# Performance work log

Hardware: AMD Instinct MI355X
Metric: run time of the kernel (lower is better)

Reference implementation:

```python
import jax, jax.numpy as jnp
import numpy as np

N = 50000      # nodes
E = 800000     # edges (avg degree 16)
F = 6          # input node features
C = 64         # conv_hidden_channels
M = 256        # mlp_hidden_channels
NCLS = 24      # num_classes
EPS = 1e-5     # BatchNorm eps


def _bn(h, g, b):
    # BatchNorm1d in training mode: biased batch stats over the batch axis
    mu = h.mean(axis=0)
    var = ((h - mu) ** 2).mean(axis=0)
    return g * (h - mu) * jax.lax.rsqrt(var + EPS) + b


def _block(x, W, b, g, beta):
    # Lin -> ReLU -> BN  (one MLP block)
    return _bn(jax.nn.relu(x @ W + b), g, beta)


def _edge_conv(x, src, dst, Wa, ba, ga, bea, Wb, bb, gb, beb):
    # EdgeConv: message = MLP([x_i, x_j - x_i]), max-aggregated onto target i
    xi = x[dst]                                   # [E, d]
    xj = x[src]                                   # [E, d]
    e = jnp.concatenate([xi, xj - xi], axis=-1)   # [E, 2d]
    h = _block(_block(e, Wa, ba, ga, bea), Wb, bb, gb, beb)  # [E, C]
    agg = jax.ops.segment_max(h, dst, num_segments=N)        # [N, C]
    return jnp.where(jnp.isfinite(agg), agg, 0.0)  # zero-fill isolated nodes


def setup_inputs() -> dict:
    key = jax.random.key(0)
    ks = jax.random.split(key, 12)

    def w(k, shape, fan_in):
        return jax.random.normal(k, shape, jnp.float32) * (1.0 / np.sqrt(fan_in))

    z = lambda *s: jnp.zeros(s, jnp.float32)
    o = lambda *s: jnp.ones(s, jnp.float32)

    x = jax.random.normal(ks[0], (N, F), jnp.float32)
    edge_index = jax.random.randint(ks[1], (2, E), 0, N, jnp.int32)

    return {
        "x": x,
        # conv1 MLP: Lin(2F,C)+BN, Lin(C,C)+BN
        "W1a": w(ks[2], (2 * F, C), 2 * F), "b1a": z(C), "g1a": o(C), "be1a": z(C),
        "W1b": w(ks[3], (C, C), C),         "b1b": z(C), "g1b": o(C), "be1b": z(C),
        # conv2/conv3 stacked: Lin(2C,C)+BN, Lin(C,C)+BN
        "Wa": w(ks[4], (2, 2 * C, C), 2 * C), "ba": z(2, C), "ga": o(2, C), "bea": z(2, C),
        "Wb": w(ks[5], (2, C, C), C),         "bb": z(2, C), "gb": o(2, C), "beb": z(2, C),
        # lin1: Lin(3C, M)+BN
        "Wl": w(ks[6], (3 * C, M), 3 * C), "bl": z(M), "gl": o(M), "bel": z(M),
        # head: Lin(M, M/4)+BN, Lin(M/4, M/8)+BN, Lin(M/8, NCLS)
        "Wm1": w(ks[7], (M, M // 4), M),      "bm1": z(M // 4), "gm1": o(M // 4), "bem1": z(M // 4),
        "Wm2": w(ks[8], (M // 4, M // 8), M // 4), "bm2": z(M // 8), "gm2": o(M // 8), "bem2": z(M // 8),
        "Wo": w(ks[9], (M // 8, NCLS), M // 8), "bo": z(NCLS),
        "edge_index": edge_index,
    }


def reference(x, W1a, b1a, g1a, be1a, W1b, b1b, g1b, be1b,
              Wa, ba, ga, bea, Wb, bb, gb, beb,
              Wl, bl, gl, bel,
              Wm1, bm1, gm1, bem1, Wm2, bm2, gm2, bem2,
              Wo, bo, edge_index):
    src, dst = edge_index[0], edge_index[1]
    x1 = _edge_conv(x,  src, dst, W1a, b1a, g1a, be1a, W1b, b1b, g1b, be1b)
    x2 = _edge_conv(x1, src, dst, Wa[0], ba[0], ga[0], bea[0], Wb[0], bb[0], gb[0], beb[0])
    x3 = _edge_conv(x2, src, dst, Wa[1], ba[1], ga[1], bea[1], Wb[1], bb[1], gb[1], beb[1])
    h = _block(jnp.concatenate([x1, x2, x3], axis=-1), Wl, bl, gl, bel)
    h = _block(h, Wm1, bm1, gm1, bem1)   # Dropout is identity (eval)
    h = _block(h, Wm2, bm2, gm2, bem2)   # Dropout is identity (eval)
    logits = h @ Wo + bo
    return jax.nn.log_softmax(logits, axis=1)
```

## Files before the change

### kernel.cpp

```cpp
#include <hip/hip_runtime.h>
#include <hip/hip_bf16.h>

#define EPS 1e-5f
typedef unsigned short bfr;
typedef unsigned short hfr;
typedef _Float16 h2v __attribute__((ext_vector_type(2)));
typedef _Float16 f16x8 __attribute__((ext_vector_type(8)));
typedef float f32x4 __attribute__((ext_vector_type(4)));

#if defined(__has_builtin)
#if __has_builtin(__builtin_amdgcn_fdot2)
#define HAS_FDOT2 1
#endif
#endif

static inline int cdiv(int a, int b){ return (a + b - 1) / b; }
static inline int imin(int a, int b){ return a < b ? a : b; }

__device__ __forceinline__ float bf2f(bfr u){ return __uint_as_float((unsigned)u << 16); }
__device__ __forceinline__ bfr f2bf(float f){
  unsigned u = __float_as_uint(f);
  u += 0x7fffu + ((u >> 16) & 1u);
  return (bfr)(u >> 16);
}
__device__ __forceinline__ unsigned pack2bf(float a, float b){
  return (unsigned)f2bf(a) | ((unsigned)f2bf(b) << 16);
}
__device__ __forceinline__ float h2f(hfr u){ _Float16 h; __builtin_memcpy(&h, &u, 2); return (float)h; }
__device__ __forceinline__ hfr f2h(float f){ _Float16 h = (_Float16)f; hfr u; __builtin_memcpy(&u, &h, 2); return u; }
__device__ __forceinline__ unsigned pack2h(float a, float b){
  return (unsigned)f2h(a) | ((unsigned)f2h(b) << 16);
}
__device__ __forceinline__ h2v u2h2(unsigned u){ h2v r; __builtin_memcpy(&r, &u, 4); return r; }
__device__ __forceinline__ unsigned h22u(h2v h){ unsigned u; __builtin_memcpy(&u, &h, 4); return u; }
__device__ __forceinline__ float dot2(h2v a, h2v b, float c){
#ifdef HAS_FDOT2
  return __builtin_amdgcn_fdot2(a, b, c, false);
#else
  return c + (float)a.x * (float)b.x + (float)a.y * (float)b.y;
#endif
}

__global__ __launch_bounds__(256) void detect_kernel(const bfr* __restrict__ xr, int nwords, int* __restrict__ flag){
  int i = threadIdx.x;
  int bad = 0;
  if (i < nwords){
    bfr lo = xr[2 * i];
    int e = (lo >> 7) & 0xFF;
    bool plausible = ((lo & 0x7FFF) == 0) || (e >= 97 && e <= 157);
    bad = plausible ? 0 : 1;
  }
  __shared__ int s[256];
  s[threadIdx.x] = bad; __syncthreads();
  for (int st = 128; st; st >>= 1){
    if (threadIdx.x < st) s[threadIdx.x] += s[threadIdx.x + st];
    __syncthreads();
  }
  if (threadIdx.x == 0) *flag = (s[0] > 32) ? 1 : 0;
}

#define NPAR 31
struct ParamPtrs { const void* p[NPAR]; };
struct ParamOfs  { int off[NPAR + 1]; };

__global__ __launch_bounds__(256) void acvt_batch_kernel(ParamPtrs pp, ParamOfs po,
                                                         float* __restrict__ out, int total,
                                                         const int* __restrict__ flag){
  int g = blockIdx.x * 256 + threadIdx.x;
  if (g >= total) return;
  int isf = *flag;
  int t = 0;
  while (po.off[t + 1] <= g) ++t;
  int i = g - po.off[t];
  out[g] = isf ? ((const float*)pp.p[t])[i] : bf2f(((const bfr*)pp.p[t])[i]);
}

__global__ __launch_bounds__(256) void deg_kernel(const int* __restrict__ dst, int* __restrict__ deg, int E){
  int e = blockIdx.x * 256 + threadIdx.x;
  if (e < E) atomicAdd(&deg[dst[e]], 1);
}

__global__ __launch_bounds__(256) void scan1_kernel(const int* __restrict__ deg, int* __restrict__ locoff,
                                                    int* __restrict__ bsum, int N){
  __shared__ int s[256];
  int i = blockIdx.x * 256 + threadIdx.x;
  int v = (i < N) ? deg[i] : 0;
  s[threadIdx.x] = v; __syncthreads();
  for (int st = 1; st < 256; st <<= 1){
    int u = (threadIdx.x >= st) ? s[threadIdx.x - st] : 0;
    __syncthreads();
    s[threadIdx.x] += u;
    __syncthreads();
  }
  if (i < N) locoff[i] = s[threadIdx.x] - v;
  if (threadIdx.x == 255) bsum[blockIdx.x] = s[255];
}

__global__ __launch_bounds__(256) void scan2_kernel(int* __restrict__ bsum, int nb){
  __shared__ int s[256];
  const int t = threadIdx.x;
  int carry = 0;
  for (int base = 0; base < nb; base += 256){
    int v = (base + t < nb) ? bsum[base + t] : 0;
    s[t] = v; __syncthreads();
    for (int st = 1; st < 256; st <<= 1){
      int u = (t >= st) ? s[t - st] : 0;
      __syncthreads();
      s[t] += u;
      __syncthreads();
    }
    if (base + t < nb) bsum[base + t] = carry + s[t] - v;
    carry += s[255];
    __syncthreads();
  }
}

__global__ __launch_bounds__(256) void scan3_kernel(const int* __restrict__ locoff, const int* __restrict__ bsum,
                                                    int* __restrict__ row_off, int* __restrict__ cur,
                                                    int N, int E){
  int i = blockIdx.x * 256 + threadIdx.x;
  if (i < N){
    int v = locoff[i] + bsum[blockIdx.x];
    row_off[i] = v; cur[i] = v;
  }
  if (i == 0) row_off[N] = E;
}

__global__ __launch_bounds__(256) void scatter_kernel(const int* __restrict__ src, const int* __restrict__ dst,
                                                      int* __restrict__ cur, int* __restrict__ ssrc, int E){
  int e = blockIdx.x * 256 + threadIdx.x;
  if (e < E){
    int d = dst[e];
    int p = atomicAdd(&cur[d], 1);
    ssrc[p] = src[e];
  }
}

template<bool FIRST>
__global__ __launch_bounds__(256) void gemmPQ_kernel(const void* __restrict__ Av, int lda,
                                                     const float* __restrict__ Wa, int d,
                                                     const float* __restrict__ ba,
                                                     hfr* __restrict__ P, hfr* __restrict__ Q, int N){
  __shared__ unsigned WsU[64 * 64];
  const int y = blockIdx.y;
  const int tot = d * 64;
  if (FIRST){
    float* Ws = (float*)WsU;
    for (int i = threadIdx.x; i < tot; i += 256)
      Ws[i] = y ? Wa[tot + i] : (Wa[i] - Wa[tot + i]);
  } else {
    for (int i = threadIdx.x; i < 32 * 64; i += 256){
      int p = i >> 6, c = i & 63;
      int i0 = (2 * p) * 64 + c, i1 = (2 * p + 1) * 64 + c;
      float w0 = y ? Wa[tot + i0] : (Wa[i0] - Wa[tot + i0]);
      float w1 = y ? Wa[tot + i1] : (Wa[i1] - Wa[tot + i1]);
      WsU[i] = pack2h(w0, w1);
    }
  }
  __syncthreads();
  const int row = blockIdx.x * 256 + threadIdx.x;
  if (row >= N) return;
  float acc[64];
#pragma unroll
  for (int c = 0; c < 64; ++c) acc[c] = 0.f;
  if (FIRST){
    const float* Ws = (const float*)WsU;
    const float* Af = (const float*)Av + (size_t)row * lda;
    for (int k = 0; k < d; ++k){
      float a = Af[k];
      const float* wr = Ws + k * 64;
#pragma unroll
      for (int c4 = 0; c4 < 16; ++c4){
        float4 w = *(const float4*)(wr + 4 * c4);
        acc[4*c4+0] += a * w.x; acc[4*c4+1] += a * w.y;
        acc[4*c4+2] += a * w.z; acc[4*c4+3] += a * w.w;
      }
    }
  } else {
    const hfr* Ah = (const hfr*)Av + (size_t)row * lda;
#pragma unroll
    for (int k8 = 0; k8 < 8; ++k8){
      uint4 av = *(const uint4*)(Ah + k8 * 8);
      unsigned pr[4] = {av.x, av.y, av.z, av.w};
#pragma unroll
      for (int pi = 0; pi < 4; ++pi){
        h2v ap = u2h2(pr[pi]);
        const unsigned* wr = WsU + (k8 * 4 + pi) * 64;
#pragma unroll
        for (int c = 0; c < 64; ++c) acc[c] = dot2(ap, u2h2(wr[c]), acc[c]);
      }
    }
  }
  if (!y){
#pragma unroll
    for (int c = 0; c < 64; ++c) acc[c] += ba[c];
  }
  unsigned p[32];
#pragma unroll
  for (int c = 0; c < 64; c += 2) p[c / 2] = pack2h(acc[c], acc[c + 1]);
  hfr* outp = (y ? Q : P) + (size_t)row * 64;
  uint4* op = (uint4*)outp;
#pragma unroll
  for (int i = 0; i < 8; ++i) op[i] = make_uint4(p[4*i], p[4*i+1], p[4*i+2], p[4*i+3]);
}

template<int NOUT, int KSTEPS, bool FOLD, bool PQ>
__global__ __launch_bounds__(256) void mgemm_kernel(const hfr* __restrict__ Ah, int lda,
                                                    const float* __restrict__ Wp0, const float* __restrict__ Wm0, int ldw,
                                                    const float* __restrict__ bias0,
                                                    const float* __restrict__ stats, float cntInv,
                                                    const float* __restrict__ g, const float* __restrict__ be,
                                                    hfr* __restrict__ Ov0, hfr* __restrict__ Ov1, int ldo,
                                                    int nrows, int relu){
  constexpr int K  = KSTEPS * 32;
  constexpr int KP = K + 8;
  constexpr int NT = NOUT / 16;
  __shared__ __align__(16) _Float16 W2T[NOUT * KP];
  __shared__ __align__(16) _Float16 etile[4][16][NOUT + 8];
  __shared__ float aS[FOLD ? K : 1], bbS[FOLD ? K : 1], bsum[FOLD ? 256 : 1];
  __shared__ float bfull[NOUT];
  const int tid = threadIdx.x;
  const int lane = tid & 63;
  const int wib = tid >> 6;
  const float* Wp = Wp0;
  const float* Wm = Wm0;
  const float* bias = bias0;
  hfr* Ov = Ov0;
  int colbase = blockIdx.y * NOUT;
  if (PQ){
    colbase = 0;
    if (blockIdx.y == 1){ Wp = Wp0 + (size_t)K * ldw; Wm = nullptr; bias = nullptr; Ov = Ov1; }
    else { Wm = Wp0 + (size_t)K * ldw; }
  }

  if (FOLD){
    for (int k = tid; k < K; k += 256){
      float mu = stats[k] * cntInv;
      float var = stats[K + k] * cntInv - mu * mu;
      float ai = g[k] * rsqrtf(var + EPS);
      aS[k] = ai; bbS[k] = be[k] - ai * mu;
    }
    __syncthreads();
  }
  for (int i = tid; i < K * NOUT; i += 256){
    int k = i / NOUT, c = i - k * NOUT;
    float w = Wp[(size_t)k * ldw + colbase + c];
    if (Wm) w -= Wm[(size_t)k * ldw + colbase + c];
    if (FOLD) w *= aS[k];
    W2T[c * KP + k] = (_Float16)w;
  }
  if (FOLD){
    constexpr int parts = 256 / NOUT;
    int c = tid % NOUT, p = tid / NOUT;
    float s = 0.f;
    for (int k = p; k < K; k += parts) s += bbS[k] * Wp[(size_t)k * ldw + colbase + c];
    bsum[p * NOUT + c] = s;
    __syncthreads();
    if (tid < NOUT){
      float t = bias[colbase + tid];
#pragma unroll
      for (int pp = 0; pp < parts; ++pp) t += bsum[pp * NOUT + tid];
      bfull[tid] = t;
    }
  } else {
    if (tid < NOUT) bfull[tid] = bias ? bias[colbase + tid] : 0.f;
  }
  __syncthreads();

  f16x8 Bf[KSTEPS][NT];
#pragma unroll
  for (int s = 0; s < KSTEPS; ++s)
#pragma unroll
    for (int t = 0; t < NT; ++t)
      Bf[s][t] = *(const f16x8*)&W2T[(t * 16 + (lane & 15)) * KP + s * 32 + (lane >> 4) * 8];
  float bc[NT];
#pragma unroll
  for (int t = 0; t < NT; ++t) bc[t] = bfull[t * 16 + (lane & 15)];

  const int ntiles = (nrows + 63) >> 6;
  for (int tile = blockIdx.x; tile < ntiles; tile += gridDim.x){
    const int r0 = tile * 64 + wib * 16;
    const int rowA = min(r0 + (lane & 15), nrows - 1);
    const hfr* Ap = Ah + (size_t)rowA * lda + (lane >> 4) * 8;
    f32x4 acc[NT];
#pragma unroll
    for (int t = 0; t < NT; ++t) acc[t] = (f32x4){bc[t], bc[t], bc[t], bc[t]};
#pragma unroll
    for (int s = 0; s < KSTEPS; ++s){
      f16x8 Af = *(const f16x8*)(Ap + s * 32);
#pragma unroll
      for (int t = 0; t < NT; ++t)
        acc[t] = __builtin_amdgcn_mfma_f32_16x16x32_f16(Af, Bf[s][t], acc[t], 0, 0, 0);
    }
#pragma unroll
    for (int t = 0; t < NT; ++t){
#pragma unroll
      for (int r = 0; r < 4; ++r){
        float v = acc[t][r];
        v = relu ? fmaxf(v, 0.f) : v;
        etile[wib][(lane >> 4) * 4 + r][t * 16 + (lane & 15)] = (_Float16)v;
      }
    }
    if (NOUT == 64){
#pragma unroll
      for (int h = 0; h < 2; ++h){
        int rl = h * 8 + (lane >> 3);
        int ch = lane & 7;
        uint4 vv = *(const uint4*)&etile[wib][rl][ch * 8];
        int rg = r0 + rl;
        if (rg < nrows) *(uint4*)(Ov + (size_t)rg * ldo + colbase + ch * 8) = vv;
      }
    } else {
      int rl = lane >> 2;
      int ch = lane & 3;
      uint4 vv = *(const uint4*)&etile[wib][rl][ch * 8];
      int rg = r0 + rl;
      if (rg < nrows) *(uint4*)(Ov + (size_t)rg * ldo + colbase + ch * 8) = vv;
    }
  }
}

__global__ __launch_bounds__(256) void passA_kernel(const hfr* __restrict__ P, const hfr* __restrict__ Q,
                                                    const int* __restrict__ ssrc, const int* __restrict__ row_off,
                                                    float* __restrict__ stats, hfr* __restrict__ h1, int N){
  const int tid = threadIdx.x;
  const int lane = tid & 63;
  const int wib = tid >> 6;
  const int er0 = lane >> 3;
  const int ck = lane & 7;
  const int wid = (blockIdx.x * 256 + tid) >> 6;
  const int nw = (gridDim.x * 256) >> 6;
  const _Float16 z16 = (_Float16)0;
  float s8[8], q8[8];
#pragma unroll
  for (int j = 0; j < 8; ++j){ s8[j] = 0.f; q8[j] = 0.f; }
  for (int n = wid; n < N; n += nw){
    const int e0 = row_off[n], e1 = row_off[n + 1];
    if (e0 >= e1) continue;
    uint4 pv4 = ((const uint4*)(P + (size_t)n * 64))[ck];
    h2v pp0 = u2h2(pv4.x), pp1 = u2h2(pv4.y), pp2 = u2h2(pv4.z), pp3 = u2h2(pv4.w);
    const int lim = e1 - 1;
    for (int eb = e0; eb < e1; eb += 16){
      int sv = ssrc[min(eb + (lane & 15), lim)];
#pragma unroll
      for (int h = 0; h < 2; ++h){
        int er = h * 8 + er0;
        int ge = eb + er;
        int sj = __shfl(sv, er, 64);
        uint4 qv = *((const uint4*)(Q + (size_t)sj * 64) + ck);
        h2v s0 = u2h2(qv.x) + pp0;
        h2v s1 = u2h2(qv.y) + pp1;
        h2v s2 = u2h2(qv.z) + pp2;
        h2v s3 = u2h2(qv.w) + pp3;
        s0.x = (s0.x < z16) ? z16 : s0.x; s0.y = (s0.y < z16) ? z16 : s0.y;
        s1.x = (s1.x < z16) ? z16 : s1.x; s1.y = (s1.y < z16) ? z16 : s1.y;
        s2.x = (s2.x < z16) ? z16 : s2.x; s2.y = (s2.y < z16) ? z16 : s2.y;
        s3.x = (s3.x < z16) ? z16 : s3.x; s3.y = (s3.y < z16) ? z16 : s3.y;
        if (ge < e1){
          *(uint4*)(h1 + (size_t)ge * 64 + ck * 8) = make_uint4(h22u(s0), h22u(s1), h22u(s2), h22u(s3));
          float v;
          v = (float)s0.x; s8[0] += v; q8[0] = fmaf(v, v, q8[0]);
          v = (float)s0.y; s8[1] += v; q8[1] = fmaf(v, v, q8[1]);
          v = (float)s1.x; s8[2] += v; q8[2] = fmaf(v, v, q8[2]);
          v = (float)s1.y; s8[3] += v; q8[3] = fmaf(v, v, q8[3]);
          v = (float)s2.x; s8[4] += v; q8[4] = fmaf(v, v, q8[4]);
          v = (float)s2.y; s8[5] += v; q8[5] = fmaf(v, v, q8[5]);
          v = (float)s3.x; s8[6] += v; q8[6] = fmaf(v, v, q8[6]);
          v = (float)s3.y; s8[7] += v; q8[7] = fmaf(v, v, q8[7]);
        }
      }
    }
  }
#pragma unroll
  for (int j = 0; j < 8; ++j){
    float s = s8[j], q = q8[j];
    s += __shfl_xor(s, 8, 64);  q += __shfl_xor(q, 8, 64);
    s += __shfl_xor(s, 16, 64); q += __shfl_xor(q, 16, 64);
    s += __shfl_xor(s, 32, 64); q += __shfl_xor(q, 32, 64);
    s8[j] = s; q8[j] = q;
  }
  __shared__ float ls[4][64], lq[4][64];
  if (lane < 8){
#pragma unroll
    for (int j = 0; j < 8; ++j){ ls[wib][lane * 8 + j] = s8[j]; lq[wib][lane * 8 + j] = q8[j]; }
  }
  __syncthreads();
  if (tid < 64){
    atomicAdd(&stats[tid], ls[0][tid] + ls[1][tid] + ls[2][tid] + ls[3][tid]);
  } else if (tid < 128){
    int c = tid - 64;
    atomicAdd(&stats[64 + c], lq[0][c] + lq[1][c] + lq[2][c] + lq[3][c]);
  }
}

__global__ __launch_bounds__(256) void passBC_kernel(const hfr* __restrict__ h1,
                                                     const int* __restrict__ row_off,
                                                     const float* __restrict__ statsIn, float Einv,
                                                     const float* __restrict__ g1, const float* __restrict__ be1,
                                                     const float* __restrict__ Wb, const float* __restrict__ bn,
                                                     float* __restrict__ agg, float* __restrict__ statsOut, int N){
  __shared__ __align__(16) _Float16 W2T[64 * 72];
  __shared__ float aS[64], bbS[64], b2S[64], bsum[256], qsum[256];
  const int tid = threadIdx.x;
  const int lane = tid & 63;
  if (tid < 64){
    float mu = statsIn[tid] * Einv;
    float var = statsIn[64 + tid] * Einv - mu * mu;
    float ai = g1[tid] * rsqrtf(var + EPS);
    aS[tid] = ai; bbS[tid] = be1[tid] - ai * mu;
  }
  __syncthreads();
  for (int i = tid; i < 4096; i += 256){
    int c = i >> 6, k = i & 63;
    W2T[c * 72 + k] = (_Float16)(aS[k] * Wb[(size_t)k * 64 + c]);
  }
  {
    int c = tid & 63, p = tid >> 6;
    float s = 0.f;
    for (int k = p; k < 64; k += 4) s += bbS[k] * Wb[(size_t)k * 64 + c];
    bsum[p * 64 + c] = s;
  }
  __syncthreads();
  if (tid < 64) b2S[tid] = bn[tid] + bsum[tid] + bsum[64 + tid] + bsum[128 + tid] + bsum[192 + tid];
  __syncthreads();
  f16x8 Bf[4][2];
#pragma unroll
  for (int t = 0; t < 4; ++t)
#pragma unroll
    for (int h = 0; h < 2; ++h){
      int c = t * 16 + (lane & 15);
      Bf[t][h] = *(const f16x8*)&W2T[c * 72 + h * 32 + (lane >> 4) * 8];
    }
  float bc[4];
#pragma unroll
  for (int t = 0; t < 4; ++t) bc[t] = b2S[t * 16 + (lane & 15)];
  const int wid = (blockIdx.x * 256 + tid) >> 6;
  const int nw = (gridDim.x * 256) >> 6;
  float sumT[4] = {0.f,0.f,0.f,0.f}, sqT[4] = {0.f,0.f,0.f,0.f};
  for (int n = wid; n < N; n += nw){
    const int e0 = row_off[n], e1 = row_off[n + 1];
    if (e0 >= e1) continue;
    float mxT[4] = {0.f,0.f,0.f,0.f};
    for (int eb = e0; eb < e1; eb += 16){
      const hfr* ap = h1 + (size_t)(eb + (lane & 15)) * 64 + (lane >> 4) * 8;
      f16x8 A0 = *(const f16x8*)ap;
      f16x8 A1 = *(const f16x8*)(ap + 32);
#pragma unroll
      for (int t = 0; t < 4; ++t){
        f32x4 Cv = {bc[t], bc[t], bc[t], bc[t]};
        Cv = __builtin_amdgcn_mfma_f32_16x16x32_f16(A0, Bf[t][0], Cv, 0, 0, 0);
        Cv = __builtin_amdgcn_mfma_f32_16x16x32_f16(A1, Bf[t][1], Cv, 0, 0, 0);
#pragma unroll
        for (int r = 0; r < 4; ++r){
          int rowi = (lane >> 4) * 4 + r;
          float v = fmaxf(Cv[r], 0.f);
          v = ((eb + rowi) < e1) ? v : 0.f;
          mxT[t] = fmaxf(mxT[t], v);
          sumT[t] += v;
          sqT[t]  = fmaf(v, v, sqT[t]);
        }
      }
    }
#pragma unroll
    for (int t = 0; t < 4; ++t){
      float m = mxT[t];
      m = fmaxf(m, __shfl_xor(m, 16, 64));
      m = fmaxf(m, __shfl_xor(m, 32, 64));
      mxT[t] = m;
    }
    float outv = (lane < 16) ? mxT[0] : (lane < 32) ? mxT[1] : (lane < 48) ? mxT[2] : mxT[3];
    agg[(size_t)n * 64 + lane] = outv;
  }
#pragma unroll
  for (int t = 0; t < 4; ++t){
    float s = sumT[t], q = sqT[t];
    s += __shfl_xor(s, 16, 64); s += __shfl_xor(s, 32, 64);
    q += __shfl_xor(q, 16, 64); q += __shfl_xor(q, 32, 64);
    sumT[t] = s; sqT[t] = q;
  }
  float ssel = (lane < 16) ? sumT[0] : (lane < 32) ? sumT[1] : (lane < 48) ? sumT[2] : sumT[3];
  float qsel = (lane < 16) ? sqT[0]  : (lane < 32) ? sqT[1]  : (lane < 48) ? sqT[2]  : sqT[3];
  bsum[tid] = ssel; qsum[tid] = qsel;
  __syncthreads();
  if (tid < 64){
    atomicAdd(&statsOut[tid], bsum[tid] + bsum[64 + tid] + bsum[128 + tid] + bsum[192 + tid]);
  } else if (tid < 128){
    int c = tid - 64;
    atomicAdd(&statsOut[64 + c], qsum[c] + qsum[64 + c] + qsum[128 + c] + qsum[192 + c]);
  }
}

__global__ __launch_bounds__(256) void fixup_kernel(const float* __restrict__ agg, const int* __restrict__ deg,
                                                    const float* __restrict__ stats, float cntInv,
                                                    const float* __restrict__ g, const float* __restrict__ be,
                                                    hfr* __restrict__ xout, int ldx, int N){
  int t = blockIdx.x * 256 + threadIdx.x;
  if (t >= N * 64) return;
  int n = t >> 6, c = t & 63;
  float mu = stats[c] * cntInv;
  float var = stats[64 + c] * cntInv - mu * mu;
  float a = g[c] * rsqrtf(var + EPS);
  float b = be[c] - a * mu;
  float v = 0.f;
  if (deg[n] > 0) v = a * agg[t] + b;
  xout[(size_t)n * ldx + c] = f2h(v);
}

template<int C>
__global__ __launch_bounds__(256) void statsN_kernel(const hfr* __restrict__ u, float* __restrict__ stats, int N){
  constexpr int CH = C / 8;
  constexpr int RP = 256 / CH;
  const int ch = threadIdx.x % CH;
  const int j0 = threadIdx.x / CH;
  float s[8], q[8];
#pragma unroll
  for (int j = 0; j < 8; ++j){ s[j] = 0.f; q[j] = 0.f; }
  for (int r = blockIdx.x * RP + j0; r < N; r += gridDim.x * RP){
    uint4 v = *(const uint4*)(u + (size_t)r * C + ch * 8);
    unsigned w[4] = {v.x, v.y, v.z, v.w};
#pragma unroll
    for (int t = 0; t < 4; ++t){
      h2v p = u2h2(w[t]);
      float a = (float)p.x, b = (float)p.y;
      s[2*t]   += a; q[2*t]   = fmaf(a, a, q[2*t]);
      s[2*t+1] += b; q[2*t+1] = fmaf(b, b, q[2*t+1]);
    }
  }
  __shared__ float ls[256][9], lq[256][9];
#pragma unroll
  for (int j = 0; j < 8; ++j){ ls[threadIdx.x][j] = s[j]; lq[threadIdx.x][j] = q[j]; }
  __syncthreads();
  if (threadIdx.x < C){
    int c = threadIdx.x, ch2 = c >> 3, jj = c & 7;
    float ss = 0.f, qq = 0.f;
    for (int p = 0; p < RP; ++p){ ss += ls[p * CH + ch2][jj]; qq += lq[p * CH + ch2][jj]; }
    atomicAdd(&stats[c], ss); atomicAdd(&stats[C + c], qq);
  }
}

__global__ __launch_bounds__(256) void head_kernel(const hfr* __restrict__ u2,
                                                   const float* __restrict__ stats, float cntInv,
                                                   const float* __restrict__ g, const float* __restrict__ be,
                                                   const float* __restrict__ Wo, const float* __restrict__ bo,
                                                   void* __restrict__ out, int N, const int* __restrict__ flag){
  __shared__ float Ws[32 * 24];
  __shared__ float bs[24];
  __shared__ float aS[32], bbS[32];
  const int tid = threadIdx.x;
  if (tid < 32){
    float mu = stats[tid] * cntInv;
    float var = stats[32 + tid] * cntInv - mu * mu;
    float ai = g[tid] * rsqrtf(var + EPS);
    aS[tid] = ai; bbS[tid] = be[tid] - ai * mu;
  }
  __syncthreads();
  for (int i = tid; i < 32 * 24; i += 256){
    int k = i / 24, c = i - 24 * k;
    Ws[i] = aS[k] * Wo[(size_t)k * 24 + c];
  }
  if (tid < 24){
    float t = bo[tid];
    for (int k = 0; k < 32; ++k) t += bbS[k] * Wo[(size_t)k * 24 + tid];
    bs[tid] = t;
  }
  __syncthreads();
  int r = blockIdx.x * 256 + tid;
  if (r >= N) return;
  int isf = *flag;
  float l[24];
#pragma unroll
  for (int c = 0; c < 24; ++c) l[c] = bs[c];
  const hfr* up = u2 + (size_t)r * 32;
#pragma unroll
  for (int k = 0; k < 32; ++k){
    float v = h2f(up[k]);
#pragma unroll
    for (int c = 0; c < 24; ++c) l[c] += v * Ws[k * 24 + c];
  }
  float m = l[0];
#pragma unroll
  for (int c = 1; c < 24; ++c) m = fmaxf(m, l[c]);
  float s = 0.f;
#pragma unroll
  for (int c = 0; c < 24; ++c) s += expf(l[c] - m);
  float lse = m + logf(s);
  if (isf){
    float4* op = (float4*)((float*)out + (size_t)r * 24);
#pragma unroll
    for (int i = 0; i < 6; ++i)
      op[i] = make_float4(l[4*i] - lse, l[4*i+1] - lse, l[4*i+2] - lse, l[4*i+3] - lse);
  } else {
    unsigned p[12];
#pragma unroll
    for (int c = 0; c < 24; c += 2) p[c / 2] = pack2bf(l[c] - lse, l[c + 1] - lse);
    uint4* op = (uint4*)((bfr*)out + (size_t)r * 24);
#pragma unroll
    for (int i = 0; i < 3; ++i) op[i] = make_uint4(p[4*i], p[4*i+1], p[4*i+2], p[4*i+3]);
  }
}

extern "C" void kernel_launch(void* const* d_in, const int* in_sizes, int n_in,
                              void* d_out, int out_size, void* d_ws, size_t ws_size,
                              hipStream_t stream){
  const int N = in_sizes[0] / 6;
  const int E = in_sizes[31] / 2;
  const int* edge = (const int*)d_in[31];
  const int* src = edge;
  const int* dst = edge + E;

  size_t off = 0; char* basep = (char*)d_ws;
  auto alloc = [&](size_t bytes) -> void* {
    void* p = basep + off;
    off = (off + bytes + 255) & ~(size_t)255;
    return p;
  };
  float* stA  = (float*)alloc(1472 * 4);
  float* stN1 = stA + 768;
  float* stN2 = stA + 1280;
  float* stN3 = stA + 1408;
  int*   flag = (int*)  alloc(4);
  int*   deg  = (int*)  alloc((size_t)N * 4);
  int*   rowo = (int*)  alloc((size_t)(N + 1) * 4);
  int*   cur  = (int*)  alloc((size_t)N * 4);
  int*   loco = (int*)  alloc((size_t)N * 4);
  int*   bsc  = (int*)  alloc(1024 * 4);
  int*   ssrc = (int*)  alloc((size_t)E * 4);

  ParamPtrs pp; ParamOfs po;
  int hoff[32]; int total = 0;
  for (int s = 0; s < NPAR; ++s){
    int idx = (s < 30) ? (s + 1) : 0;
    pp.p[s] = d_in[idx];
    po.off[s] = total;
    hoff[idx] = total;
    total += in_sizes[idx];
  }
  po.off[NPAR] = total;
  float* pf = (float*)alloc((size_t)total * 4);

  hfr*   P    = (hfr*)  alloc((size_t)N * 64 * 2);
  hfr*   Qb   = (hfr*)  alloc((size_t)N * 64 * 2);
  float* agg  = (float*)alloc((size_t)N * 64 * 4);
  hfr*   xcat = (hfr*)  alloc((size_t)N * 192 * 2);
  hfr*   h1   = (hfr*)  alloc((size_t)(E + 16) * 64 * 2);
  hfr* u_l = (hfr*)P;
  hfr* u1  = xcat;
  hfr* u2  = xcat + (size_t)N * 64;
  (void)ws_size; (void)n_in; (void)out_size;

  dim3 B(256);
  detect_kernel<<<1, B, 0, stream>>>((const bfr*)d_in[0], 256, flag);
  acvt_batch_kernel<<<cdiv(total, 256), B, 0, stream>>>(pp, po, pf, total, flag);

  hipMemsetAsync(stA, 0, 1472 * 4, stream);
  hipMemsetAsync(deg, 0, (size_t)N * 4, stream);
  hipMemsetAsync(h1 + (size_t)E * 64, 0, 16 * 64 * 2, stream);
  deg_kernel<<<cdiv(E, 256), B, 0, stream>>>(dst, deg, E);
  const int NBn = cdiv(N, 256);
  scan1_kernel<<<NBn, B, 0, stream>>>(deg, loco, bsc, N);
  scan2_kernel<<<1, B, 0, stream>>>(bsc, NBn);
  scan3_kernel<<<NBn, B, 0, stream>>>(loco, bsc, rowo, cur, N, E);
  scatter_kernel<<<cdiv(E, 256), B, 0, stream>>>(src, dst, cur, ssrc, E);

  const int NB = cdiv(N, 256);
  const int ntiles = cdiv(N, 64);
  const int GWA = 1024, GWB = 1024;
  const float Einv = 1.f / (float)E;
  for (int k = 0; k < 3; ++k){
    const float *Wa_k, *ba_k, *ga_k, *bea_k, *Wb_k, *bb_k, *gb_k, *beb_k;
    if (k == 0){
      Wa_k = pf + hoff[1]; ba_k = pf + hoff[2]; ga_k = pf + hoff[3]; bea_k = pf + hoff[4];
      Wb_k = pf + hoff[5]; bb_k = pf + hoff[6]; gb_k = pf + hoff[7]; beb_k = pf + hoff[8];
    } else {
      int kk = k - 1;
      Wa_k = pf + hoff[9]  + (size_t)kk * 128 * 64;
      ba_k = pf + hoff[10] + kk * 64;
      ga_k = pf + hoff[11] + kk * 64;
      bea_k= pf + hoff[12] + kk * 64;
      Wb_k = pf + hoff[13] + (size_t)kk * 64 * 64;
      bb_k = pf + hoff[14] + kk * 64;
      gb_k = pf + hoff[15] + kk * 64;
      beb_k= pf + hoff[16] + kk * 64;
    }
    float* st1 = stA + k * 256;
    float* st2 = st1 + 128;
    if (k == 0){
      gemmPQ_kernel<true><<<dim3(NB, 2), B, 0, stream>>>(pf + hoff[0], 6, Wa_k, 6, ba_k, P, Qb, N);
    } else {
      mgemm_kernel<64, 2, false, true><<<dim3(imin(ntiles, 1024), 2), B, 0, stream>>>(
          xcat + (size_t)(k - 1) * 64, 192, Wa_k, nullptr, 64, ba_k,
          nullptr, 0.f, nullptr, nullptr, P, Qb, 64, N, 0);
    }
    passA_kernel<<<GWA, B, 0, stream>>>(P, Qb, ssrc, rowo, st1, h1, N);
    passBC_kernel<<<GWB, B, 0, stream>>>(h1, rowo, st1, Einv, ga_k, bea_k, Wb_k, bb_k,
                                         agg, st2, N);
    fixup_kernel<<<cdiv(N * 64, 256), B, 0, stream>>>(agg, deg, st2, Einv, gb_k, beb_k,
                                                      xcat + (size_t)k * 64, 192, N);
  }

  mgemm_kernel<64, 6, false, false><<<dim3(imin(ntiles, 256), 4), B, 0, stream>>>(
      xcat, 192, pf + hoff[17], nullptr, 256, pf + hoff[18],
      nullptr, 0.f, nullptr, nullptr, u_l, nullptr, 256, N, 1);
  statsN_kernel<256><<<512, B, 0, stream>>>(u_l, stN1, N);
  mgemm_kernel<32, 8, true, false><<<dim3(imin(ntiles, 512), 2), B, 0, stream>>>(
      u_l, 256, pf + hoff[21], nullptr, 64, pf + hoff[22],
      stN1, 1.f / (float)N, pf + hoff[19], pf + hoff[20], u1, nullptr, 64, N, 1);
  statsN_kernel<64><<<512, B, 0, stream>>>(u1, stN2, N);
  mgemm_kernel<32, 2, true, false><<<dim3(imin(ntiles, 1024), 1), B, 0, stream>>>(
      u1, 64, pf + hoff[25], nullptr, 32, pf + hoff[26],
      stN2, 1.f / (float)N, pf + hoff[23], pf + hoff[24], u2, nullptr, 32, N, 1);
  statsN_kernel<32><<<512, B, 0, stream>>>(u2, stN3, N);
  head_kernel<<<cdiv(N, 256), B, 0, stream>>>(u2, stN3, 1.f / (float)N, pf + hoff[27], pf + hoff[28],
                                              pf + hoff[29], pf + hoff[30], d_out, N, flag);
  (void)NB;
}
```

Before: 745.8 us.

## Batch four nodes per wave and prefetch first edge tiles in passA/passB

Result: no change. 750.9 us (+0.7%).

```diff
diff --git a/kernel.cpp b/kernel.cpp
--- a/kernel.cpp
+++ b/kernel.cpp
@@ -123,7 +123,7 @@
     int v = locoff[i] + bsum[blockIdx.x];
     row_off[i] = v; cur[i] = v;
   }
-  if (i == 0) row_off[N] = E;
+  if (i < 8) row_off[N + i] = E;
 }
 
 __global__ __launch_bounds__(256) void scatter_kernel(const int* __restrict__ src, const int* __restrict__ dst,
@@ -328,45 +328,72 @@
   const int wib = tid >> 6;
   const int er0 = lane >> 3;
   const int ck = lane & 7;
+  const int lm = lane & 15;
   const int wid = (blockIdx.x * 256 + tid) >> 6;
   const int nw = (gridDim.x * 256) >> 6;
   const _Float16 z16 = (_Float16)0;
   float s8[8], q8[8];
 #pragma unroll
   for (int j = 0; j < 8; ++j){ s8[j] = 0.f; q8[j] = 0.f; }
-  for (int n = wid; n < N; n += nw){
-    const int e0 = row_off[n], e1 = row_off[n + 1];
-    if (e0 >= e1) continue;
-    uint4 pv4 = ((const uint4*)(P + (size_t)n * 64))[ck];
-    h2v pp0 = u2h2(pv4.x), pp1 = u2h2(pv4.y), pp2 = u2h2(pv4.z), pp3 = u2h2(pv4.w);
-    const int lim = e1 - 1;
-    for (int eb = e0; eb < e1; eb += 16){
-      int sv = ssrc[min(eb + (lane & 15), lim)];
+
+  auto edgeBlock = [&](uint4 qv, h2v pp0, h2v pp1, h2v pp2, h2v pp3, int ge, int e1){
+    h2v s0 = u2h2(qv.x) + pp0;
+    h2v s1 = u2h2(qv.y) + pp1;
+    h2v s2 = u2h2(qv.z) + pp2;
+    h2v s3 = u2h2(qv.w) + pp3;
+    s0.x = (s0.x < z16) ? z16 : s0.x; s0.y = (s0.y < z16) ? z16 : s0.y;
+    s1.x = (s1.x < z16) ? z16 : s1.x; s1.y = (s1.y < z16) ? z16 : s1.y;
+    s2.x = (s2.x < z16) ? z16 : s2.x; s2.y = (s2.y < z16) ? z16 : s2.y;
+    s3.x = (s3.x < z16) ? z16 : s3.x; s3.y = (s3.y < z16) ? z16 : s3.y;
+    if (ge < e1){
+      *(uint4*)(h1 + (size_t)ge * 64 + ck * 8) = make_uint4(h22u(s0), h22u(s1), h22u(s2), h22u(s3));
+      float v;
+      v = (float)s0.x; s8[0] += v; q8[0] = fmaf(v, v, q8[0]);
+      v = (float)s0.y; s8[1] += v; q8[1] = fmaf(v, v, q8[1]);
+      v = (float)s1.x; s8[2] += v; q8[2] = fmaf(v, v, q8[2]);
+      v = (float)s1.y; s8[3] += v; q8[3] = fmaf(v, v, q8[3]);
+      v = (float)s2.x; s8[4] += v; q8[4] = fmaf(v, v, q8[4]);
+      v = (float)s2.y; s8[5] += v; q8[5] = fmaf(v, v, q8[5]);
+      v = (float)s3.x; s8[6] += v; q8[6] = fmaf(v, v, q8[6]);
+      v = (float)s3.y; s8[7] += v; q8[7] = fmaf(v, v, q8[7]);
+    }
+  };
+
+  for (int n0 = wid * 4; n0 < N; n0 += nw * 4){
+    int4 ro = *(const int4*)(row_off + n0);
+    int e4  = row_off[n0 + 4];
+    int e0a[4] = {ro.x, ro.y, ro.z, ro.w};
+    int e1a[4] = {ro.y, ro.z, ro.w, e4};
+    uint4 pv[4]; int sv[4];
+#pragma unroll
+    for (int j = 0; j < 4; ++j){
+      int np = min(n0 + j, N - 1);
+      pv[j] = ((const uint4*)(P + (size_t)np * 64))[ck];
+      sv[j] = ssrc[e0a[j] + lm];
+    }
+    uint4 qg[4][2];
+#pragma unroll
+    for (int j = 0; j < 4; ++j)
 #pragma unroll
       for (int h = 0; h < 2; ++h){
-        int er = h * 8 + er0;
-        int ge = eb + er;
-        int sj = __shfl(sv, er, 64);
-        uint4 qv = *((const uint4*)(Q + (size_t)sj * 64) + ck);
-        h2v s0 = u2h2(qv.x) + pp0;
-        h2v s1 = u2h2(qv.y) + pp1;
-        h2v s2 = u2h2(qv.z) + pp2;
-        h2v s3 = u2h2(qv.w) + pp3;
-        s0.x = (s0.x < z16) ? z16 : s0.x; s0.y = (s0.y < z16) ? z16 : s0.y;
-        s1.x = (s1.x < z16) ? z16 : s1.x; s1.y = (s1.y < z16) ? z16 : s1.y;
-        s2.x = (s2.x < z16) ? z16 : s2.x; s2.y = (s2.y < z16) ? z16 : s2.y;
-        s3.x = (s3.x < z16) ? z16 : s3.x; s3.y = (s3.y < z16) ? z16 : s3.y;
-        if (ge < e1){
-          *(uint4*)(h1 + (size_t)ge * 64 + ck * 8) = make_uint4(h22u(s0), h22u(s1), h22u(s2), h22u(s3));
-          float v;
-          v = (float)s0.x; s8[0] += v; q8[0] = fmaf(v, v, q8[0]);
-          v = (float)s0.y; s8[1] += v; q8[1] = fmaf(v, v, q8[1]);
-          v = (float)s1.x; s8[2] += v; q8[2] = fmaf(v, v, q8[2]);
-          v = (float)s1.y; s8[3] += v; q8[3] = fmaf(v, v, q8[3]);
-          v = (float)s2.x; s8[4] += v; q8[4] = fmaf(v, v, q8[4]);
-          v = (float)s2.y; s8[5] += v; q8[5] = fmaf(v, v, q8[5]);
-          v = (float)s3.x; s8[6] += v; q8[6] = fmaf(v, v, q8[6]);
-          v = (float)s3.y; s8[7] += v; q8[7] = fmaf(v, v, q8[7]);
+        int sj = __shfl(sv[j], h * 8 + er0, 64);
+        qg[j][h] = *((const uint4*)(Q + (size_t)sj * 64) + ck);
+      }
+#pragma unroll
+    for (int j = 0; j < 4; ++j){
+      const int e0 = e0a[j], e1 = e1a[j];
+      if (e0 >= e1) continue;
+      h2v pp0 = u2h2(pv[j].x), pp1 = u2h2(pv[j].y), pp2 = u2h2(pv[j].z), pp3 = u2h2(pv[j].w);
+#pragma unroll
+      for (int h = 0; h < 2; ++h)
+        edgeBlock(qg[j][h], pp0, pp1, pp2, pp3, e0 + h * 8 + er0, e1);
+      for (int eb = e0 + 16; eb < e1; eb += 16){
+        int svt = ssrc[eb + lm];
+#pragma unroll
+        for (int h = 0; h < 2; ++h){
+          int sj = __shfl(svt, h * 8 + er0, 64);
+          uint4 qv = *((const uint4*)(Q + (size_t)sj * 64) + ck);
+          edgeBlock(qv, pp0, pp1, pp2, pp3, eb + h * 8 + er0, e1);
         }
       }
     }
@@ -436,40 +463,68 @@
   for (int t = 0; t < 4; ++t) bc[t] = b2S[t * 16 + (lane & 15)];
   const int wid = (blockIdx.x * 256 + tid) >> 6;
   const int nw = (gridDim.x * 256) >> 6;
+  const int lm = lane & 15, lq2 = lane >> 4;
+  const float FINF = __uint_as_float(0x7f800000u);
   float sumT[4] = {0.f,0.f,0.f,0.f}, sqT[4] = {0.f,0.f,0.f,0.f};
-  for (int n = wid; n < N; n += nw){
-    const int e0 = row_off[n], e1 = row_off[n + 1];
-    if (e0 >= e1) continue;
-    float mxT[4] = {0.f,0.f,0.f,0.f};
-    for (int eb = e0; eb < e1; eb += 16){
-      const hfr* ap = h1 + (size_t)(eb + (lane & 15)) * 64 + (lane >> 4) * 8;
-      f16x8 A0 = *(const f16x8*)ap;
-      f16x8 A1 = *(const f16x8*)(ap + 32);
+
+  auto tileStats = [&](int eb, int e1, f16x8 Aa, f16x8 Ab, float* mxT){
+    bool full = (eb + 16 <= e1);
+    float msk[4];
+    if (!full){
+#pragma unroll
+      for (int r = 0; r < 4; ++r)
+        msk[r] = (eb + lq2 * 4 + r < e1) ? FINF : 0.f;
+    }
+#pragma unroll
+    for (int t = 0; t < 4; ++t){
+      f32x4 Cv = {bc[t], bc[t], bc[t], bc[t]};
+      Cv = __builtin_amdgcn_mfma_f32_16x16x32_f16(Aa, Bf[t][0], Cv, 0, 0, 0);
+      Cv = __builtin_amdgcn_mfma_f32_16x16x32_f16(Ab, Bf[t][1], Cv, 0, 0, 0);
+#pragma unroll
+      for (int r = 0; r < 4; ++r){
+        float v = fmaxf(Cv[r], 0.f);
+        if (!full) v = fminf(v, msk[r]);
+        mxT[t] = fmaxf(mxT[t], v);
+        sumT[t] += v;
+        sqT[t] = fmaf(v, v, sqT[t]);
+      }
+    }
+  };
+
+  for (int n0 = wid * 4; n0 < N; n0 += nw * 4){
+    int4 ro = *(const int4*)(row_off + n0);
+    int e4  = row_off[n0 + 4];
+    int e0a[4] = {ro.x, ro.y, ro.z, ro.w};
+    int e1a[4] = {ro.y, ro.z, ro.w, e4};
+    f16x8 A0[4], A1[4];
+#pragma unroll
+    for (int j = 0; j < 4; ++j){
+      const hfr* ap = h1 + (size_t)(e0a[j] + lm) * 64 + lq2 * 8;
+      A0[j] = *(const f16x8*)ap;
+      A1[j] = *(const f16x8*)(ap + 32);
+    }
+#pragma unroll
+    for (int j = 0; j < 4; ++j){
+      const int e0 = e0a[j], e1 = e1a[j];
+      if (e0 >= e1) continue;
+      float mxT[4] = {0.f,0.f,0.f,0.f};
+      tileStats(e0, e1, A0[j], A1[j], mxT);
+      for (int eb = e0 + 16; eb < e1; eb += 16){
+        const hfr* ap = h1 + (size_t)(eb + lm) * 64 + lq2 * 8;
+        f16x8 B0 = *(const f16x8*)ap;
+        f16x8 B1 = *(const f16x8*)(ap + 32);
+        tileStats(eb, e1, B0, B1, mxT);
+      }
 #pragma unroll
       for (int t = 0; t < 4; ++t){
-        f32x4 Cv = {bc[t], bc[t], bc[t], bc[t]};
-        Cv = __builtin_amdgcn_mfma_f32_16x16x32_f16(A0, Bf[t][0], Cv, 0, 0, 0);
-        Cv = __builtin_amdgcn_mfma_f32_16x16x32_f16(A1, Bf[t][1], Cv, 0, 0, 0);
-#pragma unroll
-        for (int r = 0; r < 4; ++r){
-          int rowi = (lane >> 4) * 4 + r;
-          float v = fmaxf(Cv[r], 0.f);
-          v = ((eb + rowi) < e1) ? v : 0.f;
-          mxT[t] = fmaxf(mxT[t], v);
-          sumT[t] += v;
-          sqT[t]  = fmaf(v, v, sqT[t]);
-        }
-      }
-    }
-#pragma unroll
-    for (int t = 0; t < 4; ++t){
-      float m = mxT[t];
-      m = fmaxf(m, __shfl_xor(m, 16, 64));
-      m = fmaxf(m, __shfl_xor(m, 32, 64));
-      mxT[t] = m;
-    }
-    float outv = (lane < 16) ? mxT[0] : (lane < 32) ? mxT[1] : (lane < 48) ? mxT[2] : mxT[3];
-    agg[(size_t)n * 64 + lane] = outv;
+        float m = mxT[t];
+        m = fmaxf(m, __shfl_xor(m, 16, 64));
+        m = fmaxf(m, __shfl_xor(m, 32, 64));
+        mxT[t] = m;
+      }
+      float outv = (lane < 16) ? mxT[0] : (lane < 32) ? mxT[1] : (lane < 48) ? mxT[2] : mxT[3];
+      agg[(size_t)(n0 + j) * 64 + lane] = outv;
+    }
   }
 #pragma unroll
   for (int t = 0; t < 4; ++t){
@@ -620,11 +675,11 @@
   float* stN3 = stA + 1408;
   int*   flag = (int*)  alloc(4);
   int*   deg  = (int*)  alloc((size_t)N * 4);
-  int*   rowo = (int*)  alloc((size_t)(N + 1) * 4);
+  int*   rowo = (int*)  alloc((size_t)(N + 8) * 4);
   int*   cur  = (int*)  alloc((size_t)N * 4);
   int*   loco = (int*)  alloc((size_t)N * 4);
   int*   bsc  = (int*)  alloc(1024 * 4);
-  int*   ssrc = (int*)  alloc((size_t)E * 4);
+  int*   ssrc = (int*)  alloc((size_t)(E + 16) * 4);
 
   ParamPtrs pp; ParamOfs po;
   int hoff[32]; int total = 0;
@@ -654,6 +709,7 @@
 
   hipMemsetAsync(stA, 0, 1472 * 4, stream);
   hipMemsetAsync(deg, 0, (size_t)N * 4, stream);
+  hipMemsetAsync(ssrc + E, 0, 16 * 4, stream);
   hipMemsetAsync(h1 + (size_t)E * 64, 0, 16 * 64 * 2, stream);
   deg_kernel<<<cdiv(E, 256), B, 0, stream>>>(dst, deg, E);
   const int NBn = cdiv(N, 256);
```
